# Kernel optimization log

Hardware: AMD Instinct MI355X
Metric: run time of the kernel (lower is better)

Reference implementation:

```python
import jax, jax.numpy as jnp
import numpy as np

DIM = 512
HEADS = 8
HEAD_DIM = DIM // HEADS
EPS = 1e-6
LN_EPS = 1e-5


def setup_inputs() -> dict:
    key = jax.random.key(0)
    ks = jax.random.split(key, 7)
    B, S = 2, 2048
    std = 1.0 / np.sqrt(DIM)
    return {
        "x": jax.random.normal(ks[0], (B, S, DIM), dtype=jnp.float32),
        "Wq": jax.random.normal(ks[1], (DIM, DIM), dtype=jnp.float32) * std,
        "Wk": jax.random.normal(ks[2], (DIM, DIM), dtype=jnp.float32) * std,
        "Wv": jax.random.normal(ks[3], (DIM, DIM), dtype=jnp.float32) * std,
        "Wo": jax.random.normal(ks[4], (DIM, DIM), dtype=jnp.float32) * std,
        "ln_gamma": jnp.ones((DIM,), dtype=jnp.float32),
        "ln_beta": jnp.zeros((DIM,), dtype=jnp.float32),
    }


def _hardsigmoid(x):
    return jnp.clip(x / 6.0 + 0.5, 0.0, 1.0)


def _softshrink(x, lambd=0.5):
    return jnp.where(x > lambd, x - lambd, jnp.where(x < -lambd, x + lambd, 0.0))


def reference(x, Wq, Wk, Wv, Wo, ln_gamma, ln_beta):
    B, S, D = x.shape
    # torch Linear: y = x @ W.T
    q = (x @ Wq.T).reshape(B, S, HEADS, HEAD_DIM).transpose(0, 2, 1, 3)
    k = (x @ Wk.T).reshape(B, S, HEADS, HEAD_DIM).transpose(0, 2, 1, 3)
    v = (x @ Wv.T).reshape(B, S, HEADS, HEAD_DIM).transpose(0, 2, 1, 3)
    scale = 1.0 / np.sqrt(HEAD_DIM)
    scores = jnp.einsum("bhqd,bhkd->bhqk", q, k) * scale  # [B,H,S,S]
    attn_soft = jax.nn.softmax(scores, axis=-1)
    gated = attn_soft * _hardsigmoid(scores)
    attn_weights = gated / (gated.sum(axis=-1, keepdims=True) + EPS)
    attn_out = jnp.einsum("bhqk,bhkd->bhqd", attn_weights, v)
    attn_out = attn_out.transpose(0, 2, 1, 3).reshape(B, S, D)
    out = attn_out @ Wo.T
    out = out / (1.0 + jnp.abs(out))  # softsign
    out = out + _softshrink(x)
    # LayerNorm over last dim
    mu = out.mean(axis=-1, keepdims=True)
    var = ((out - mu) ** 2).mean(axis=-1, keepdims=True)
    out = (out - mu) * jax.lax.rsqrt(var + LN_EPS) * ln_gamma + ln_beta
    return out
```

## Files before the change

### kernel.cpp

```cpp
#include <hip/hip_runtime.h>

#define DIMD 512
#define NB 2
#define SEQ 2048
#define NHEADS 8
#define HDIM 64
#define MROWS (NB*SEQ)

typedef short s16x8 __attribute__((ext_vector_type(8)));
typedef float f32x4 __attribute__((ext_vector_type(4)));
typedef float f32x16 __attribute__((ext_vector_type(16)));
typedef unsigned short u16;
typedef unsigned int u32;

__device__ __forceinline__ u16 f2bf(float f) {
    union { float f; u32 u; } c; c.f = f;
    u32 u = c.u;
    return (u16)((u + 0x7FFFu + ((u >> 16) & 1u)) >> 16);
}
__device__ __forceinline__ float bf2f(u16 v) {
    union { u32 u; float f; } c; c.u = ((u32)v) << 16;
    return c.f;
}

__device__ __forceinline__ f32x4 mfma16(s16x8 a, s16x8 b, f32x4 c) {
    return __builtin_amdgcn_mfma_f32_16x16x32_bf16(a, b, c, 0, 0, 0);
}
__device__ __forceinline__ f32x16 mfma32(s16x8 a, s16x8 b, f32x16 c) {
    return __builtin_amdgcn_mfma_f32_32x32x16_bf16(a, b, c, 0, 0, 0);
}
__device__ __forceinline__ float fexp2(float x) {
    float r; asm("v_exp_f32 %0, %1" : "=v"(r) : "v"(x)); return r;
}
__device__ __forceinline__ float frcp(float x) {
    float r; asm("v_rcp_f32 %0, %1" : "=v"(r) : "v"(x)); return r;
}

#define GLDS16(g, l) __builtin_amdgcn_global_load_lds( \
    (const __attribute__((address_space(1))) void*)(g), \
    (__attribute__((address_space(3))) void*)(l), 16, 0, 0)

#define ESCF 0.180336880111f
#define HSC2 0.115524530f

__global__ void cvt_all(const float* __restrict__ x, const float* __restrict__ Wq,
                        const float* __restrict__ Wk, const float* __restrict__ Wv,
                        const float* __restrict__ Wo,
                        u16* __restrict__ xb, u16* __restrict__ wqkv, u16* __restrict__ wo) {
    int i = blockIdx.x * blockDim.x + threadIdx.x;
    const float* src; u16* dst; int idx;
    if (i < 524288) { src = x; dst = xb; idx = i; }
    else {
        int jj = i - 524288;
        int which = jj >> 16; idx = jj & 65535;
        src = which == 0 ? Wq : which == 1 ? Wk : which == 2 ? Wv : Wo;
        dst = which < 3 ? wqkv + which*DIMD*DIMD : wo;
    }
    float4 v = reinterpret_cast<const float4*>(src)[idx];
    ushort4 o;
    o.x = f2bf(v.x); o.y = f2bf(v.y); o.z = f2bf(v.z); o.w = f2bf(v.w);
    reinterpret_cast<ushort4*>(dst)[idx] = o;
}

template<int WMODE>
__global__ __launch_bounds__(256) void gemm128x64(const u16* __restrict__ A, const u16* __restrict__ Bm,
                                                  void* __restrict__ Cout, void* __restrict__ Cout2,
                                                  void* __restrict__ Cout3, int M, int N, int K) {
    __shared__ u16 As[128*64];
    __shared__ u16 Bs[64*64];
    const int bm0 = blockIdx.x * 128, bn0 = blockIdx.y * 64;
    const int t = threadIdx.x;
    const int w = t >> 6, l = t & 63;
    const int lg = l >> 4, lr = l & 15;
    f32x4 acc[2][4] = {};
    const int sr8 = l >> 3;
    const int swc = ((l & 7) ^ (sr8 & 7)) * 8;
    const int arow = w*32 + sr8;
    const int brow = w*8 + sr8;
    const u16* asrc = A  + (size_t)(bm0 + arow)*K + swc;
    const u16* bsrc = Bm + (size_t)(bn0 + brow)*K + swc;

    for (int k0 = 0; k0 < K; k0 += 64) {
        #pragma unroll
        for (int g = 0; g < 4; g++)
            GLDS16(asrc + (size_t)g*8*K + k0, &As[w*2048 + g*512]);
        #pragma unroll
        for (int g = 0; g < 2; g++)
            GLDS16(bsrc + (size_t)g*32*K + k0, &Bs[g*2048 + w*512]);
        __syncthreads();
        #pragma unroll
        for (int ks = 0; ks < 2; ks++) {
            const int swr = ((ks*4 + lg) ^ (lr & 7)) * 8;
            s16x8 af[2], bfr[4];
            #pragma unroll
            for (int fm = 0; fm < 2; fm++)
                af[fm] = *(const s16x8*)&As[(w*32 + fm*16 + lr)*64 + swr];
            #pragma unroll
            for (int fn = 0; fn < 4; fn++)
                bfr[fn] = *(const s16x8*)&Bs[(fn*16 + lr)*64 + swr];
            #pragma unroll
            for (int fm = 0; fm < 2; fm++)
                #pragma unroll
                for (int fn = 0; fn < 4; fn++)
                    acc[fm][fn] = mfma16(af[fm], bfr[fn], acc[fm][fn]);
        }
        __syncthreads();
    }

    const int region = (WMODE == 3) ? (bn0 >> 9) : 0;
    const float qsc = (WMODE == 3 && region == 0) ? ESCF : 1.0f;
    #pragma unroll
    for (int fm = 0; fm < 2; fm++) {
        #pragma unroll
        for (int fn = 0; fn < 4; fn++) {
            const int mb = bm0 + w*32 + fm*16 + lg*4;
            const int n  = bn0 + fn*16 + lr;
            if (WMODE == 2) {
                float* C = (float*)Cout;
                #pragma unroll
                for (int i = 0; i < 4; i++)
                    C[(size_t)(mb + i)*N + n] = acc[fm][fn][i];
            } else {
                const int nl = n & 511;
                if (region == 2) {
                    const int b = mb >> 11, s0 = mb & 2047;
                    const int h = nl >> 6, d = nl & 63;
                    ushort4 pk;
                    pk.x = f2bf(acc[fm][fn][0]);
                    pk.y = f2bf(acc[fm][fn][1]);
                    pk.z = f2bf(acc[fm][fn][2]);
                    pk.w = f2bf(acc[fm][fn][3]);
                    *(ushort4*)((u16*)Cout3 + (size_t)((b*8 + h)*64 + d)*2048 + s0) = pk;
                } else {
                    u16* C = region == 0 ? (u16*)Cout : (u16*)Cout2;
                    #pragma unroll
                    for (int i = 0; i < 4; i++)
                        C[(size_t)(mb + i)*512 + nl] = f2bf(acc[fm][fn][i] * qsc);
                }
            }
        }
    }
}

__global__ __launch_bounds__(256) void gemm_bt2f(const u16* __restrict__ opart,
                                                 const float* __restrict__ gpart,
                                                 const u16* __restrict__ Bm,
                                                 u16* __restrict__ Cout) {
    __shared__ u16 As[32*64];
    __shared__ u16 Bs[64*64];
    __shared__ float ginv[32][9];
    const int bm0 = blockIdx.x * 32, bn0 = blockIdx.y * 64;
    const int t = threadIdx.x;
    const int w = t >> 6, l = t & 63;
    const int lg = l >> 4, lr = l & 15;
    const int wm = w >> 1, wn = w & 1;
    f32x4 acc[2] = {};
    const int srow = t >> 3;
    const int c8 = t & 7;
    const int scol = c8 * 8;
    const int swz = (c8 ^ (srow & 7)) * 8;

    {
        const int r = t >> 3, h = t & 7;
        const int rg = bm0 + r;
        const int b = rg >> 11, s = rg & 2047;
        float g = gpart[(size_t)(b*8 + h)*SEQ + s]
                + gpart[(size_t)(16 + b*8 + h)*SEQ + s]
                + gpart[(size_t)(32 + b*8 + h)*SEQ + s]
                + gpart[(size_t)(48 + b*8 + h)*SEQ + s];
        ginv[r][h] = frcp(g);
    }
    __syncthreads();

    for (int k0 = 0; k0 < DIMD; k0 += 64) {
        const int h = k0 >> 6;
        #pragma unroll
        for (int c = 0; c < 2; c++) {
            const u16* gb = Bm + (size_t)(bn0 + c*32 + srow)*DIMD + k0 + swz;
            GLDS16(gb, (char*)Bs + c*4096 + w*1024);
        }
        {
            const int rl = srow;
            const int rg = bm0 + rl;
            const u16* oprow = opart + (size_t)rg*DIMD + k0 + scol;
            s16x8 p0 = *(const s16x8*)(oprow);
            s16x8 p1 = *(const s16x8*)(oprow + (size_t)MROWS*DIMD);
            s16x8 p2 = *(const s16x8*)(oprow + (size_t)2*MROWS*DIMD);
            s16x8 p3 = *(const s16x8*)(oprow + (size_t)3*MROWS*DIMD);
            const float inv = ginv[rl][h];
            union { u32 uu[4]; s16x8 v; } av;
            #pragma unroll
            for (int e2 = 0; e2 < 4; e2++) {
                const float s0 = (bf2f((u16)p0[2*e2]) + bf2f((u16)p1[2*e2]))
                               + (bf2f((u16)p2[2*e2]) + bf2f((u16)p3[2*e2]));
                const float s1 = (bf2f((u16)p0[2*e2+1]) + bf2f((u16)p1[2*e2+1]))
                               + (bf2f((u16)p2[2*e2+1]) + bf2f((u16)p3[2*e2+1]));
                asm("v_cvt_pk_bf16_f32 %0, %1, %2" : "=v"(av.uu[e2]) : "v"(s0*inv), "v"(s1*inv));
            }
            *(s16x8*)&As[rl*64 + swz] = av.v;
        }
        __syncthreads();
        #pragma unroll
        for (int ks = 0; ks < 2; ks++) {
            const int rc = ((ks*4 + lg) ^ (lr & 7)) * 8;
            s16x8 af = *(const s16x8*)&As[(wm*16 + lr)*64 + rc];
            s16x8 bfr[2];
            #pragma unroll
            for (int fn = 0; fn < 2; fn++)
                bfr[fn] = *(const s16x8*)&Bs[(wn*32 + fn*16 + lr)*64 + rc];
            #pragma unroll
            for (int fn = 0; fn < 2; fn++)
                acc[fn] = mfma16(af, bfr[fn], acc[fn]);
        }
        __syncthreads();
    }

    #pragma unroll
    for (int fn = 0; fn < 2; fn++) {
        const int mb = bm0 + wm*16 + lg*4;
        const int n  = bn0 + wn*32 + fn*16 + lr;
        #pragma unroll
        for (int i = 0; i < 4; i++)
            Cout[(size_t)(mb + i)*DIMD + n] = f2bf(acc[fn][i]);
    }
}

__global__ __launch_bounds__(256) void attn_split(const u16* __restrict__ q, const u16* __restrict__ k,
                                                  const u16* __restrict__ vt,
                                                  u16* __restrict__ opart, float* __restrict__ gpart) {
    __shared__ u16 Ks[3][64*64];
    __shared__ u16 Vs[2][64*64];
    const int bid = blockIdx.x;
    const int xcd = bid & 7, j = bid >> 3;
    const int g8 = j >> 4, qt = j & 15;
    const int bhks = xcd*8 + g8;
    const int bh = bhks >> 2, ks = bhks & 3;
    const int b = bh >> 3, h = bh & 7;
    const int qb0 = qt * 128;
    const int t = threadIdx.x;
    const int w = t >> 6, l = t & 63;
    const int ln = l & 31, hi = l >> 5, l7 = l & 7;

    const size_t qrow = (size_t)(b*SEQ + qb0 + w*32 + ln);
    s16x8 qf[4];
    #pragma unroll
    for (int c = 0; c < 4; c++)
        qf[c] = *(const s16x8*)(q + qrow*DIMD + h*HDIM + c*16 + hi*8);

    const int sr = l >> 3;
    const int swc = ((l & 7) ^ sr) * 8;
    const u16* ksrc = k  + (size_t)(b*SEQ + ks*512 + w*16 + sr)*DIMD + h*HDIM + swc;
    const u16* vsrc = vt + (size_t)bh*HDIM*SEQ + (size_t)(w*16 + sr)*SEQ + ks*512 + swc;
    const int ldsw = w*1024;

    f32x16 o0 = {}, o1 = {};
    float gacc = 0.f;

#define SV(T, B) do { GLDS16(vsrc + (T)*64,                 &Vs[B][ldsw]); \
                      GLDS16(vsrc + (size_t)8*SEQ + (T)*64, &Vs[B][ldsw + 512]); } while(0)
#define SK(T, B) do { GLDS16(ksrc + (size_t)((T)*64)*DIMD,     &Ks[B][ldsw]); \
                      GLDS16(ksrc + (size_t)((T)*64 + 8)*DIMD, &Ks[B][ldsw + 512]); } while(0)
#define WB(N) do { asm volatile("s_waitcnt vmcnt(" #N ")" ::: "memory"); \
                   __builtin_amdgcn_s_barrier(); \
                   asm volatile("" ::: "memory"); } while(0)
#define QKH(B, KB, SC) do { SC = (f32x16){}; \
    __builtin_amdgcn_s_setprio(1); \
    _Pragma("unroll") for (int c_ = 0; c_ < 4; c_++) { \
        const int ch_ = (((c_ << 1) | hi) ^ l7) * 8; \
        s16x8 kf_ = *(const s16x8*)&Ks[B][((KB)*32 + ln)*64 + ch_]; \
        SC = mfma32(kf_, qf[c_], SC); } \
    __builtin_amdgcn_s_setprio(0); } while(0)
#define SMPV(SC, KB, VB) do { \
    u32 up_[4][2]; \
    _Pragma("unroll") for (int b2_ = 0; b2_ < 4; b2_++) { \
        const float s0_ = SC[b2_*4+0], s1_ = SC[b2_*4+1]; \
        const float s2_ = SC[b2_*4+2], s3_ = SC[b2_*4+3]; \
        const float w0_ = fexp2(s0_) * __builtin_amdgcn_fmed3f(s0_*HSC2 + 0.5f, 0.f, 1.f); \
        const float w1_ = fexp2(s1_) * __builtin_amdgcn_fmed3f(s1_*HSC2 + 0.5f, 0.f, 1.f); \
        const float w2_ = fexp2(s2_) * __builtin_amdgcn_fmed3f(s2_*HSC2 + 0.5f, 0.f, 1.f); \
        const float w3_ = fexp2(s3_) * __builtin_amdgcn_fmed3f(s3_*HSC2 + 0.5f, 0.f, 1.f); \
        gacc += (w0_ + w1_) + (w2_ + w3_); \
        asm("v_cvt_pk_bf16_f32 %0, %1, %2" : "=v"(up_[b2_][0]) : "v"(w0_), "v"(w1_)); \
        asm("v_cvt_pk_bf16_f32 %0, %1, %2" : "=v"(up_[b2_][1]) : "v"(w2_), "v"(w3_)); } \
    _Pragma("unroll") for (int c16_ = 0; c16_ < 2; c16_++) { \
        u32 x0_ = up_[2*c16_][0], y0_ = up_[2*c16_+1][0]; \
        u32 x1_ = up_[2*c16_][1], y1_ = up_[2*c16_+1][1]; \
        asm("v_permlane32_swap_b32 %0, %1" : "+v"(x0_), "+v"(y0_)); \
        asm("v_permlane32_swap_b32 %0, %1" : "+v"(x1_), "+v"(y1_)); \
        union { u32 w[4]; s16x8 v; } pa_; \
        pa_.w[0] = x0_; pa_.w[1] = x1_; pa_.w[2] = y0_; pa_.w[3] = y1_; \
        const int ccv_ = (KB)*4 + c16_*2 + hi; \
        s16x8 vf0_ = *(const s16x8*)&Vs[VB][(size_t)ln*64        + (ccv_ ^ l7)*8]; \
        s16x8 vf1_ = *(const s16x8*)&Vs[VB][(size_t)(32 + ln)*64 + (ccv_ ^ l7)*8]; \
        __builtin_amdgcn_s_setprio(1); \
        o0 = mfma32(pa_.v, vf0_, o0); \
        o1 = mfma32(pa_.v, vf1_, o1); \
        __builtin_amdgcn_s_setprio(0); } } while(0)

    f32x16 a0, a1, b0, b1;
    SV(0,0); SK(0,0); SK(1,1);
    WB(2);
    QKH(0,0,a0); SK(2,2); QKH(0,1,a1);
    WB(2);
    SV(1,1); QKH(1,0,b0); SK(3,0); SMPV(a0,0,0); QKH(1,1,b1); SMPV(a1,1,0);
    WB(2);
    SV(2,0); QKH(2,0,a0); SK(4,1); SMPV(b0,0,1); QKH(2,1,a1); SMPV(b1,1,1);
    WB(2);
    SV(3,1); QKH(0,0,b0); SK(5,2); SMPV(a0,0,0); QKH(0,1,b1); SMPV(a1,1,0);
    WB(2);
    SV(4,0); QKH(1,0,a0); SK(6,0); SMPV(b0,0,1); QKH(1,1,a1); SMPV(b1,1,1);
    WB(2);
    SV(5,1); QKH(2,0,b0); SK(7,1); SMPV(a0,0,0); QKH(2,1,b1); SMPV(a1,1,0);
    WB(2);
    SV(6,0); QKH(0,0,a0); SMPV(b0,0,1); QKH(0,1,a1); SMPV(b1,1,1);
    WB(0);
    SV(7,1); QKH(1,0,b0); SMPV(a0,0,0); QKH(1,1,b1); SMPV(a1,1,0);
    WB(0);
    SMPV(b0,0,1); SMPV(b1,1,1);

#undef SV
#undef SK
#undef WB
#undef QKH
#undef SMPV

    gacc += __shfl_xor(gacc, 32);
    if (l < 32)
        gpart[((size_t)ks*16 + bh)*SEQ + qb0 + w*32 + l] = gacc;

    u16* op = opart + ((size_t)ks*MROWS + b*SEQ + qb0 + w*32)*DIMD + h*HDIM;
    #pragma unroll
    for (int i = 0; i < 16; i++) {
        const int qr = (i & 3) + 8*(i >> 2) + 4*hi;
        op[(size_t)qr*DIMD + ln]      = f2bf(o0[i]);
        op[(size_t)qr*DIMD + 32 + ln] = f2bf(o1[i]);
    }
}

__global__ __launch_bounds__(256) void ln_epilogue(const u16* __restrict__ proj, const float* __restrict__ x,
                                                   const float* __restrict__ gamma, const float* __restrict__ beta,
                                                   float* __restrict__ out) {
    const int row = blockIdx.x*4 + (threadIdx.x >> 6);
    const int l = threadIdx.x & 63;
    const u16* pr = proj + (size_t)row*DIMD + l*8;
    const float* xr = x  + (size_t)row*DIMD + l*8;
    s16x8 pv = *(const s16x8*)pr;
    float tv[8];
    float s = 0.f, s2 = 0.f;
    #pragma unroll
    for (int j = 0; j < 2; j++) {
        float4 xv = *(const float4*)(xr + j*4);
        float xa[4] = {xv.x, xv.y, xv.z, xv.w};
        #pragma unroll
        for (int qq = 0; qq < 4; qq++) {
            const float p = bf2f((u16)pv[j*4+qq]);
            const float ss = p / (1.f + fabsf(p));
            const float xx = xa[qq];
            const float sh = xx > 0.5f ? xx - 0.5f : (xx < -0.5f ? xx + 0.5f : 0.f);
            const float tt = ss + sh;
            tv[j*4+qq] = tt; s += tt; s2 += tt*tt;
        }
    }
    #pragma unroll
    for (int m = 1; m < 64; m <<= 1) { s += __shfl_xor(s, m); s2 += __shfl_xor(s2, m); }
    const float mu = s * (1.f/512.f);
    float var = s2 * (1.f/512.f) - mu*mu;
    const float rstd = rsqrtf(var + 1e-5f);
    #pragma unroll
    for (int j = 0; j < 2; j++) {
        float4 g  = *(const float4*)(gamma + l*8 + j*4);
        float4 bb = *(const float4*)(beta  + l*8 + j*4);
        float4 ov;
        ov.x = (tv[j*4+0]-mu)*rstd*g.x + bb.x;
        ov.y = (tv[j*4+1]-mu)*rstd*g.y + bb.y;
        ov.z = (tv[j*4+2]-mu)*rstd*g.z + bb.z;
        ov.w = (tv[j*4+3]-mu)*rstd*g.w + bb.w;
        *(float4*)(out + (size_t)row*DIMD + l*8 + j*4) = ov;
    }
}

extern "C" void kernel_launch(void* const* d_in, const int* in_sizes, int n_in,
                              void* d_out, int out_size, void* d_ws, size_t ws_size,
                              hipStream_t stream) {
    const float* x     = (const float*)d_in[0];
    const float* Wq    = (const float*)d_in[1];
    const float* Wk    = (const float*)d_in[2];
    const float* Wv    = (const float*)d_in[3];
    const float* Wo    = (const float*)d_in[4];
    const float* gamma = (const float*)d_in[5];
    const float* beta  = (const float*)d_in[6];
    float* out = (float*)d_out;
    char* ws = (char*)d_ws;

    u16* xb    = (u16*)(ws);
    u16* wqkvb = (u16*)(ws + (4<<20));
    u16* wob   = (u16*)(ws + (4<<20) + (1536<<10));
    u16* qb    = (u16*)(ws + (6<<20));
    u16* kb    = (u16*)(ws + (10<<20));
    u16* vtb   = (u16*)(ws + (14<<20));
    u16* proj  = (u16*)(ws + (22<<20));
    u16* opart = (u16*)(ws + (26<<20));
    float* gpart = (float*)(ws + (42<<20));

    cvt_all<<<3072, 256, 0, stream>>>(x, Wq, Wk, Wv, Wo, xb, wqkvb, wob);

    gemm128x64<3><<<dim3(MROWS/128, 1536/64), 256, 0, stream>>>(xb, wqkvb, qb, kb, vtb, MROWS, 1536, DIMD);

    attn_split<<<1024, 256, 0, stream>>>(qb, kb, vtb, opart, gpart);

    gemm_bt2f<<<dim3(MROWS/32, DIMD/64), 256, 0, stream>>>(opart, gpart, wob, proj);

    ln_epilogue<<<MROWS/4, 256, 0, stream>>>(proj, x, gamma, beta, out);
}
```

Baseline: 63.87 us.

## Split attention keys eight ways with a matching eight-partial output projection

Adds an attention kernel that splits the key dimension into eight chunks of 256 instead of four, launching 2048 blocks to raise parallelism and shorten each block's serial loop. The output-projection GEMM is templated on the split count so it sums eight bf16 partials and eight gate-sum partials. The gpart buffer moves to make room for the larger opart buffer. The old path stays as a fallback when the workspace is too small. The cost is twice the partial-output traffic written and then read back by the projection GEMM.

```diff
diff --git a/kernel.cpp b/kernel.cpp
--- a/kernel.cpp
+++ b/kernel.cpp
@@ -142,6 +142,7 @@
     }
 }
 
+template<int NS>
 __global__ __launch_bounds__(256) void gemm_bt2f(const u16* __restrict__ opart,
                                                  const float* __restrict__ gpart,
                                                  const u16* __restrict__ Bm,
@@ -164,10 +165,10 @@
         const int r = t >> 3, h = t & 7;
         const int rg = bm0 + r;
         const int b = rg >> 11, s = rg & 2047;
-        float g = gpart[(size_t)(b*8 + h)*SEQ + s]
-                + gpart[(size_t)(16 + b*8 + h)*SEQ + s]
-                + gpart[(size_t)(32 + b*8 + h)*SEQ + s]
-                + gpart[(size_t)(48 + b*8 + h)*SEQ + s];
+        float g = 0.f;
+        #pragma unroll
+        for (int p = 0; p < NS; p++)
+            g += gpart[(size_t)(p*16 + b*8 + h)*SEQ + s];
         ginv[r][h] = frcp(g);
     }
     __syncthreads();
@@ -183,18 +184,20 @@
             const int rl = srow;
             const int rg = bm0 + rl;
             const u16* oprow = opart + (size_t)rg*DIMD + k0 + scol;
-            s16x8 p0 = *(const s16x8*)(oprow);
-            s16x8 p1 = *(const s16x8*)(oprow + (size_t)MROWS*DIMD);
-            s16x8 p2 = *(const s16x8*)(oprow + (size_t)2*MROWS*DIMD);
-            s16x8 p3 = *(const s16x8*)(oprow + (size_t)3*MROWS*DIMD);
+            s16x8 pv[NS];
+            #pragma unroll
+            for (int p = 0; p < NS; p++)
+                pv[p] = *(const s16x8*)(oprow + (size_t)p*MROWS*DIMD);
             const float inv = ginv[rl][h];
             union { u32 uu[4]; s16x8 v; } av;
             #pragma unroll
             for (int e2 = 0; e2 < 4; e2++) {
-                const float s0 = (bf2f((u16)p0[2*e2]) + bf2f((u16)p1[2*e2]))
-                               + (bf2f((u16)p2[2*e2]) + bf2f((u16)p3[2*e2]));
-                const float s1 = (bf2f((u16)p0[2*e2+1]) + bf2f((u16)p1[2*e2+1]))
-                               + (bf2f((u16)p2[2*e2+1]) + bf2f((u16)p3[2*e2+1]));
+                float s0 = 0.f, s1 = 0.f;
+                #pragma unroll
+                for (int p = 0; p < NS; p++) {
+                    s0 += bf2f((u16)pv[p][2*e2]);
+                    s1 += bf2f((u16)pv[p][2*e2+1]);
+                }
                 asm("v_cvt_pk_bf16_f32 %0, %1, %2" : "=v"(av.uu[e2]) : "v"(s0*inv), "v"(s1*inv));
             }
             *(s16x8*)&As[rl*64 + swz] = av.v;
@@ -337,6 +340,133 @@
     }
 }
 
+__device__ __forceinline__ void attn_phase64(const u16* Kc, const u16* Vc, const s16x8* qf,
+                                             f32x16& o0, f32x16& o1, float& gacc,
+                                             int ln, int hi, int l7) {
+    f32x16 sc0 = {}, sc1 = {};
+    __builtin_amdgcn_s_setprio(1);
+    #pragma unroll
+    for (int c = 0; c < 4; c++) {
+        const int ch = (((c << 1) | hi) ^ l7) * 8;
+        s16x8 kf0 = *(const s16x8*)&Kc[ln*64 + ch];
+        s16x8 kf1 = *(const s16x8*)&Kc[(32 + ln)*64 + ch];
+        sc0 = mfma32(kf0, qf[c], sc0);
+        sc1 = mfma32(kf1, qf[c], sc1);
+    }
+    __builtin_amdgcn_s_setprio(0);
+    #pragma unroll
+    for (int kb = 0; kb < 2; kb++) {
+        const f32x16& sc = kb ? sc1 : sc0;
+        u32 u[4][2];
+        #pragma unroll
+        for (int b2 = 0; b2 < 4; b2++) {
+            float ww[4];
+            #pragma unroll
+            for (int r = 0; r < 4; r++) {
+                const float s = sc[b2*4 + r];
+                const float e = fexp2(s);
+                const float hs = __builtin_amdgcn_fmed3f(s*HSC2 + 0.5f, 0.f, 1.f);
+                ww[r] = e*hs;
+            }
+            gacc += (ww[0] + ww[1]) + (ww[2] + ww[3]);
+            asm("v_cvt_pk_bf16_f32 %0, %1, %2" : "=v"(u[b2][0]) : "v"(ww[0]), "v"(ww[1]));
+            asm("v_cvt_pk_bf16_f32 %0, %1, %2" : "=v"(u[b2][1]) : "v"(ww[2]), "v"(ww[3]));
+        }
+        #pragma unroll
+        for (int c16 = 0; c16 < 2; c16++) {
+            u32 x0 = u[2*c16][0], y0 = u[2*c16+1][0];
+            u32 x1 = u[2*c16][1], y1 = u[2*c16+1][1];
+            asm("v_permlane32_swap_b32 %0, %1" : "+v"(x0), "+v"(y0));
+            asm("v_permlane32_swap_b32 %0, %1" : "+v"(x1), "+v"(y1));
+            union { u32 uu[4]; s16x8 v; } pa;
+            pa.uu[0] = x0; pa.uu[1] = x1; pa.uu[2] = y0; pa.uu[3] = y1;
+            const int ccv = kb*4 + c16*2 + hi;
+            s16x8 vf0 = *(const s16x8*)&Vc[(size_t)ln*64        + (ccv ^ l7)*8];
+            s16x8 vf1 = *(const s16x8*)&Vc[(size_t)(32 + ln)*64 + (ccv ^ l7)*8];
+            __builtin_amdgcn_s_setprio(1);
+            o0 = mfma32(pa.v, vf0, o0);
+            o1 = mfma32(pa.v, vf1, o1);
+            __builtin_amdgcn_s_setprio(0);
+        }
+    }
+}
+
+__global__ __launch_bounds__(256) void attn_split8(const u16* __restrict__ q, const u16* __restrict__ k,
+                                                   const u16* __restrict__ vt,
+                                                   u16* __restrict__ opart, float* __restrict__ gpart) {
+    __shared__ u16 Ks[2][64*64];
+    __shared__ u16 Vs[2][64*64];
+    const int bid = blockIdx.x;
+    const int xcd = bid & 7, j = bid >> 3;
+    const int g16 = j >> 4, qt = j & 15;
+    const int bhks = xcd*16 + g16;
+    const int bh = bhks >> 3, ks = bhks & 7;
+    const int b = bh >> 3, h = bh & 7;
+    const int qb0 = qt * 128;
+    const int t = threadIdx.x;
+    const int w = t >> 6, l = t & 63;
+    const int ln = l & 31, hi = l >> 5, l7 = l & 7;
+
+    const size_t qrow = (size_t)(b*SEQ + qb0 + w*32 + ln);
+    s16x8 qf[4];
+    #pragma unroll
+    for (int c = 0; c < 4; c++)
+        qf[c] = *(const s16x8*)(q + qrow*DIMD + h*HDIM + c*16 + hi*8);
+
+    const int sr = l >> 3;
+    const int swc = ((l & 7) ^ sr) * 8;
+    const u16* ksrc = k  + (size_t)(b*SEQ + ks*256 + w*16 + sr)*DIMD + h*HDIM + swc;
+    const u16* vsrc = vt + (size_t)bh*HDIM*SEQ + (size_t)(w*16 + sr)*SEQ + ks*256 + swc;
+    const int ldsw = w*1024;
+
+    f32x16 o0 = {}, o1 = {};
+    float gacc = 0.f;
+
+    #pragma unroll
+    for (int g = 0; g < 2; g++) {
+        GLDS16(ksrc + (size_t)g*8*DIMD, &Ks[0][ldsw + g*512]);
+        GLDS16(vsrc + (size_t)g*8*SEQ,  &Vs[0][ldsw + g*512]);
+    }
+    __syncthreads();
+
+    #pragma unroll 1
+    for (int tp = 0; tp < 2; ++tp) {
+        const int tt0 = tp*2;
+        {
+            const int adv = (tt0 + 1) * 64;
+            #pragma unroll
+            for (int g = 0; g < 2; g++) {
+                GLDS16(ksrc + (size_t)(adv)*DIMD + (size_t)g*8*DIMD, &Ks[1][ldsw + g*512]);
+                GLDS16(vsrc + (size_t)g*8*SEQ + adv,                 &Vs[1][ldsw + g*512]);
+            }
+        }
+        attn_phase64(&Ks[0][0], &Vs[0][0], qf, o0, o1, gacc, ln, hi, l7);
+        __syncthreads();
+        if (tp < 1) {
+            const int adv = (tt0 + 2) * 64;
+            #pragma unroll
+            for (int g = 0; g < 2; g++) {
+                GLDS16(ksrc + (size_t)(adv)*DIMD + (size_t)g*8*DIMD, &Ks[0][ldsw + g*512]);
+                GLDS16(vsrc + (size_t)g*8*SEQ + adv,                 &Vs[0][ldsw + g*512]);
+            }
+        }
+        attn_phase64(&Ks[1][0], &Vs[1][0], qf, o0, o1, gacc, ln, hi, l7);
+        __syncthreads();
+    }
+
+    gacc += __shfl_xor(gacc, 32);
+    if (l < 32)
+        gpart[((size_t)ks*16 + bh)*SEQ + qb0 + w*32 + l] = gacc;
+
+    u16* op = opart + ((size_t)ks*MROWS + b*SEQ + qb0 + w*32)*DIMD + h*HDIM;
+    #pragma unroll
+    for (int i = 0; i < 16; i++) {
+        const int qr = (i & 3) + 8*(i >> 2) + 4*hi;
+        op[(size_t)qr*DIMD + ln]      = f2bf(o0[i]);
+        op[(size_t)qr*DIMD + 32 + ln] = f2bf(o1[i]);
+    }
+}
+
 __global__ __launch_bounds__(256) void ln_epilogue(const u16* __restrict__ proj, const float* __restrict__ x,
                                                    const float* __restrict__ gamma, const float* __restrict__ beta,
                                                    float* __restrict__ out) {
@@ -398,17 +528,22 @@
     u16* qb    = (u16*)(ws + (6<<20));
     u16* kb    = (u16*)(ws + (10<<20));
     u16* vtb   = (u16*)(ws + (14<<20));
+    float* gpart = (float*)(ws + (18<<20));
     u16* proj  = (u16*)(ws + (22<<20));
     u16* opart = (u16*)(ws + (26<<20));
-    float* gpart = (float*)(ws + (42<<20));
 
     cvt_all<<<3072, 256, 0, stream>>>(x, Wq, Wk, Wv, Wo, xb, wqkvb, wob);
 
     gemm128x64<3><<<dim3(MROWS/128, 1536/64), 256, 0, stream>>>(xb, wqkvb, qb, kb, vtb, MROWS, 1536, DIMD);
 
-    attn_split<<<1024, 256, 0, stream>>>(qb, kb, vtb, opart, gpart);
-
-    gemm_bt2f<<<dim3(MROWS/32, DIMD/64), 256, 0, stream>>>(opart, gpart, wob, proj);
+    const size_t need8 = ((size_t)26 << 20) + ((size_t)32 << 20);
+    if (ws_size >= need8) {
+        attn_split8<<<2048, 256, 0, stream>>>(qb, kb, vtb, opart, gpart);
+        gemm_bt2f<8><<<dim3(MROWS/32, DIMD/64), 256, 0, stream>>>(opart, gpart, wob, proj);
+    } else {
+        attn_split<<<1024, 256, 0, stream>>>(qb, kb, vtb, opart, gpart);
+        gemm_bt2f<4><<<dim3(MROWS/32, DIMD/64), 256, 0, stream>>>(opart, gpart, wob, proj);
+    }
 
     ln_epilogue<<<MROWS/4, 256, 0, stream>>>(proj, x, gamma, beta, out);
 }
```

New measurement: 73.28 us. 14.7% more time.
